# Kernel tuning notes

Hardware: AMD Instinct MI355X
Metric: run time of the kernel (lower is better)

Reference implementation:

```python
import jax, jax.numpy as jnp
import numpy as np

LN_EPS = 1e-5
SN_EPS = 1e-12


def _block(x, W, b, g, be):
    # Linear -> LayerNorm -> CELU, fused as one expression chain
    h = x @ W.T + b
    mu = jnp.mean(h, axis=-1, keepdims=True)
    var = jnp.mean(jnp.square(h - mu), axis=-1, keepdims=True)
    h = (h - mu) * jax.lax.rsqrt(var + LN_EPS) * g + be
    return jax.nn.celu(h)


def _spectral_norm_weight(W, u):
    # One power iteration (torch training-mode behavior), u/v detached.
    v = W.T @ u
    v = v / (jnp.linalg.norm(v) + SN_EPS)
    u2 = W @ v
    u2 = u2 / (jnp.linalg.norm(u2) + SN_EPS)
    sigma = u2 @ (W @ v)
    return W / sigma


def setup_inputs() -> dict:
    key = jax.random.key(0)
    ks = jax.random.split(key, 8)
    B, D = 131072, 512
    sizes = [512, 128, 32, 8]
    inp = {"x": jax.random.normal(ks[0], (B, D), dtype=jnp.float32)}
    fan_in = D
    for i, s in enumerate(sizes, start=1):
        scale = 1.0 / np.sqrt(fan_in)
        inp[f"W{i}"] = jax.random.normal(ks[i], (s, fan_in), dtype=jnp.float32) * scale
        inp[f"b{i}"] = jnp.zeros((s,), dtype=jnp.float32)
        inp[f"g{i}"] = jnp.ones((s,), dtype=jnp.float32)
        inp[f"be{i}"] = jnp.zeros((s,), dtype=jnp.float32)
        fan_in = s
    inp["Wh"] = jax.random.normal(ks[5], (1, 8), dtype=jnp.float32) * (1.0 / np.sqrt(8))
    inp["bh"] = jnp.zeros((1,), dtype=jnp.float32)
    inp["u"] = jax.random.normal(ks[6], (1,), dtype=jnp.float32)
    return inp


def reference(x, W1, b1, g1, be1, W2, b2, g2, be2, W3, b3, g3, be3,
              W4, b4, g4, be4, Wh, bh, u):
    h = _block(x, W1, b1, g1, be1)
    h = _block(h, W2, b2, g2, be2)
    h = _block(h, W3, b3, g3, be3)
    h = _block(h, W4, b4, g4, be4)          # hidden_output: [B, 8]
    Wsn = _spectral_norm_weight(Wh, u)
    return h @ Wsn.T + bh                   # [B, 1]
```

## Files before the change

kernel.cpp:

```cpp
#include <hip/hip_runtime.h>


typedef unsigned short u16;
typedef unsigned int   u32;
typedef __bf16  bf16x8 __attribute__((ext_vector_type(8)));
typedef float   f32x16 __attribute__((ext_vector_type(16)));

__device__ __forceinline__ u16 f2bf(float f) {
    u32 x = __builtin_bit_cast(u32, f);
    x += 0x7FFFu + ((x >> 16) & 1u);
    return (u16)(x >> 16);
}
__device__ __forceinline__ float bfval(u16 h) { return __builtin_bit_cast(float, (u32)h << 16); }
__device__ __forceinline__ u32 pack2(float a, float b) { return (u32)f2bf(a) | ((u32)f2bf(b) << 16); }
__device__ __forceinline__ float celu1(float x) { return x > 0.f ? x : __expf(x) - 1.f; }

#define PB1 0
#define PG1 512
#define PBE1 1024
#define PB2 1536
#define PG2 1664
#define PBE2 1792
#define PB3 1920
#define PG3 1952
#define PBE3 1984
#define PB4 2016
#define PG4 2024
#define PBE4 2032
#define PW4 2040
#define PWH 2296
#define PBH 2304
#define PU  2305
#define NPAR 2306

#define W1F_OFF 0
#define W2F_OFF 262144
#define W3F_OFF 327680
#define W3LF_OFF 331776
#define NGROUPS 41984

__global__ void prep_weights(const float* __restrict__ W1, const float* __restrict__ W2,
                             const float* __restrict__ W3, u16* __restrict__ wsb) {
    const int g = blockIdx.x * 256 + threadIdx.x;
    if (g < 32768) {
        const int l = g & 63, t = (g >> 6) & 15, ksg = g >> 10;
        const int n = t * 32 + (l & 31);
        const int k0 = ksg * 16 + (l >> 5) * 8;
        u16* dst = wsb + W1F_OFF + g * 8;
        const float* src = W1 + n * 512 + k0;
#pragma unroll
        for (int e = 0; e < 8; ++e) dst[e] = f2bf(src[e]);
    } else if (g < 40960) {
        const int h = g - 32768;
        const int l = h & 63, t = (h >> 6) & 3, ksg = h >> 8;
        const int n = t * 32 + (l & 31);
        const int k0 = ksg * 16 + (l >> 5) * 8;
        u16* dst = wsb + W2F_OFF + h * 8;
        const float* src = W2 + n * 512 + k0;
#pragma unroll
        for (int e = 0; e < 8; ++e) dst[e] = f2bf(src[e]);
    } else if (g < 41472) {
        const int h = g - 40960;
        const int l = h & 63, ksg = h >> 6;
        const int n = l & 31;
        const int k0 = ksg * 16 + (l >> 5) * 8;
        u16* dst = wsb + W3F_OFF + h * 8;
        const float* src = W3 + n * 128 + k0;
#pragma unroll
        for (int e = 0; e < 8; ++e) dst[e] = f2bf(src[e]);
    } else {
        const int h = g - 41472;
        const int l = h & 63, ksg = h >> 6;
        const int n = l & 31;
        const int k0 = ksg * 16 + (l >> 5) * 8;
        u16* dst = wsb + W3LF_OFF + h * 8;
        const float* src = W3 + n * 128 + k0;
#pragma unroll
        for (int e = 0; e < 8; ++e) { float w = src[e]; dst[e] = f2bf(w - bfval(f2bf(w))); }
    }
}

__global__ __launch_bounds__(512, 2) void fused_mlp(
    const float* __restrict__ x,
    const u16* __restrict__ W1b, const u16* __restrict__ W2b,
    const u16* __restrict__ W3b, const u16* __restrict__ W3Lb,
    const float* __restrict__ b1, const float* __restrict__ g1, const float* __restrict__ be1,
    const float* __restrict__ b2, const float* __restrict__ g2, const float* __restrict__ be2,
    const float* __restrict__ b3, const float* __restrict__ g3, const float* __restrict__ be3,
    const float* __restrict__ W4, const float* __restrict__ b4, const float* __restrict__ g4,
    const float* __restrict__ be4,
    const float* __restrict__ Wh, const float* __restrict__ bh, const float* __restrict__ uvec,
    float* __restrict__ out)
{
    __shared__ __align__(16) u16 sA[64][72];
    __shared__ __align__(16) u16 sH1[64][520];
    __shared__ __align__(16) u16 sH2[64][136];
    __shared__ __align__(16) u16 sH2L[64][136];
    __shared__ __align__(16) float sH3f[64][36];
    __shared__ __align__(16) float sPS[64][8];
    __shared__ __align__(16) float sPQ[64][8];
    __shared__ float sMu[64], sRs[64];
    __shared__ __align__(16) float sP[NPAR + 2];

    const int tid = threadIdx.x;
    const int row0 = blockIdx.x * 64;
    const int wv = tid >> 6;
    const int lane = tid & 63;
    const int ln = lane & 31;
    const int lh = lane >> 5;

    for (int i = tid; i < NPAR; i += 512) {
        float v;
        if      (i < 512)  v = b1[i];
        else if (i < 1024) v = g1[i - 512];
        else if (i < 1536) v = be1[i - 1024];
        else if (i < 1664) v = b2[i - 1536];
        else if (i < 1792) v = g2[i - 1664];
        else if (i < 1920) v = be2[i - 1792];
        else if (i < 1952) v = b3[i - 1920];
        else if (i < 1984) v = g3[i - 1952];
        else if (i < 2016) v = be3[i - 1984];
        else if (i < 2024) v = b4[i - 2016];
        else if (i < 2032) v = g4[i - 2024];
        else if (i < 2040) v = be4[i - 2032];
        else if (i < 2296) v = W4[i - 2040];
        else if (i < 2304) v = Wh[i - 2296];
        else if (i == 2304) v = bh[0];
        else                v = uvec[0];
        sP[i] = v;
    }

    const int Mt = wv >> 2;
    const int Ng = wv & 3;

    const int sr = tid >> 3;
    const int sc = (tid & 7) * 8;
    const float* xrow = x + (long)(row0 + sr) * 512 + sc;

    float4 pa0 = *(const float4*)(xrow);
    float4 pa1 = *(const float4*)(xrow + 4);
    float4 pb0 = *(const float4*)(xrow + 64);
    float4 pb1 = *(const float4*)(xrow + 68);

    const u16* wq = W1b + (Ng * 4) * 512 + lane * 8;
    bf16x8 Bf[4][4];
#pragma unroll
    for (int s = 0; s < 3; ++s)
#pragma unroll
        for (int nt = 0; nt < 4; ++nt)
            Bf[s][nt] = *(const bf16x8*)(wq + s * 8192 + nt * 512);

    f32x16 acc[4] = {};

#pragma unroll
    for (int c = 0; c < 8; ++c) {
        __syncthreads();
        {
            float4 q0 = (c & 1) ? pb0 : pa0;
            float4 q1 = (c & 1) ? pb1 : pa1;
            uint4 wv4;
            wv4.x = pack2(q0.x, q0.y);
            wv4.y = pack2(q0.z, q0.w);
            wv4.z = pack2(q1.x, q1.y);
            wv4.w = pack2(q1.z, q1.w);
            *(uint4*)(&sA[sr][sc]) = wv4;
        }
        __syncthreads();
        if (c + 2 < 8) {
            const float* nx = xrow + (c + 2) * 64;
            if (c & 1) { pb0 = *(const float4*)(nx); pb1 = *(const float4*)(nx + 4); }
            else       { pa0 = *(const float4*)(nx); pa1 = *(const float4*)(nx + 4); }
        }
#pragma unroll
        for (int ks = 0; ks < 4; ++ks) {
            const int ksg = c * 4 + ks;
            const int slot = ksg & 3;
            if (ksg + 3 < 32) {
                const int ps = (ksg + 3) & 3;
                const u16* np = wq + (ksg + 3) * 8192;
                Bf[ps][0] = *(const bf16x8*)(np);
                Bf[ps][1] = *(const bf16x8*)(np + 512);
                Bf[ps][2] = *(const bf16x8*)(np + 1024);
                Bf[ps][3] = *(const bf16x8*)(np + 1536);
            }
            bf16x8 af = *(const bf16x8*)(&sA[Mt * 32 + ln][ks * 16 + lh * 8]);
            acc[0] = __builtin_amdgcn_mfma_f32_32x32x16_bf16(af, Bf[slot][0], acc[0], 0, 0, 0);
            acc[1] = __builtin_amdgcn_mfma_f32_32x32x16_bf16(af, Bf[slot][1], acc[1], 0, 0, 0);
            acc[2] = __builtin_amdgcn_mfma_f32_32x32x16_bf16(af, Bf[slot][2], acc[2], 0, 0, 0);
            acc[3] = __builtin_amdgcn_mfma_f32_32x32x16_bf16(af, Bf[slot][3], acc[3], 0, 0, 0);
        }
    }

#pragma unroll
    for (int nt = 0; nt < 4; ++nt) {
        const float bb = sP[PB1 + (Ng * 4 + nt) * 32 + ln];
#pragma unroll
        for (int rg = 0; rg < 16; ++rg) acc[nt][rg] += bb;
    }
#pragma unroll
    for (int rg = 0; rg < 16; ++rg) {
        float s = acc[0][rg] + acc[1][rg] + acc[2][rg] + acc[3][rg];
        float q = acc[0][rg] * acc[0][rg] + acc[1][rg] * acc[1][rg]
                + acc[2][rg] * acc[2][rg] + acc[3][rg] * acc[3][rg];
#pragma unroll
        for (int m = 1; m < 32; m <<= 1) { s += __shfl_xor(s, m, 64); q += __shfl_xor(q, m, 64); }
        if (ln == 0) {
            const int row = Mt * 32 + (rg & 3) + 8 * (rg >> 2) + 4 * lh;
            sPS[row][Ng] = s; sPQ[row][Ng] = q;
        }
    }
    __syncthreads();
    if (tid < 64) {
        float s = sPS[tid][0] + sPS[tid][1] + sPS[tid][2] + sPS[tid][3];
        float q = sPQ[tid][0] + sPQ[tid][1] + sPQ[tid][2] + sPQ[tid][3];
        const float mu = s * (1.f / 512.f);
        const float var = q * (1.f / 512.f) - mu * mu;
        sMu[tid] = mu; sRs[tid] = rsqrtf(var + 1e-5f);
    }
    __syncthreads();
    {
        float gg[4], ee[4];
#pragma unroll
        for (int nt = 0; nt < 4; ++nt) {
            const int col = (Ng * 4 + nt) * 32 + ln;
            gg[nt] = sP[PG1 + col]; ee[nt] = sP[PBE1 + col];
        }
#pragma unroll
        for (int rg = 0; rg < 16; ++rg) {
            const int row = Mt * 32 + (rg & 3) + 8 * (rg >> 2) + 4 * lh;
            const float mu = sMu[row], rs = sRs[row];
#pragma unroll
            for (int nt = 0; nt < 4; ++nt) {
                const int col = (Ng * 4 + nt) * 32 + ln;
                const float hn = (acc[nt][rg] - mu) * rs * gg[nt] + ee[nt];
                sH1[row][col] = f2bf(celu1(hn));
            }
        }
    }
    __syncthreads();

    float v2[16];
    {
        const int Mt2 = wv >> 2;
        const int Nt2 = wv & 3;
        const u16* w2q = W2b + Nt2 * 512 + lane * 8;
        bf16x8 W2f[4];
#pragma unroll
        for (int s = 0; s < 4; ++s) W2f[s] = *(const bf16x8*)(w2q + s * 2048);

        f32x16 a2 = {}, a2b = {};
        const u16* h1p = &sH1[Mt2 * 32 + ln][lh * 8];
#pragma unroll
        for (int ksg = 0; ksg < 32; ++ksg) {
            const int slot = ksg & 3;
            bf16x8 af = *(const bf16x8*)(h1p + ksg * 16);
            if (ksg & 1) a2b = __builtin_amdgcn_mfma_f32_32x32x16_bf16(af, W2f[slot], a2b, 0, 0, 0);
            else         a2  = __builtin_amdgcn_mfma_f32_32x32x16_bf16(af, W2f[slot], a2, 0, 0, 0);
            if (ksg + 4 < 32) W2f[slot] = *(const bf16x8*)(w2q + (ksg + 4) * 2048);
        }
        const float bb = sP[PB2 + Nt2 * 32 + ln];
#pragma unroll
        for (int rg = 0; rg < 16; ++rg) v2[rg] = a2[rg] + a2b[rg] + bb;
#pragma unroll
        for (int rg = 0; rg < 16; ++rg) {
            float s = v2[rg], q = v2[rg] * v2[rg];
#pragma unroll
            for (int m = 1; m < 32; m <<= 1) { s += __shfl_xor(s, m, 64); q += __shfl_xor(q, m, 64); }
            if (ln == 0) {
                const int row = Mt2 * 32 + (rg & 3) + 8 * (rg >> 2) + 4 * lh;
                sPS[row][Nt2] = s; sPQ[row][Nt2] = q;
            }
        }
    }
    __syncthreads();
    if (tid < 64) {
        float s = sPS[tid][0] + sPS[tid][1] + sPS[tid][2] + sPS[tid][3];
        float q = sPQ[tid][0] + sPQ[tid][1] + sPQ[tid][2] + sPQ[tid][3];
        const float mu = s * (1.f / 128.f);
        const float var = q * (1.f / 128.f) - mu * mu;
        sMu[tid] = mu; sRs[tid] = rsqrtf(var + 1e-5f);
    }
    __syncthreads();
    {
        const int Mt2 = wv >> 2;
        const int Nt2 = wv & 3;
        const int col = Nt2 * 32 + ln;
        const float gg = sP[PG2 + col], ee = sP[PBE2 + col];
#pragma unroll
        for (int rg = 0; rg < 16; ++rg) {
            const int row = Mt2 * 32 + (rg & 3) + 8 * (rg >> 2) + 4 * lh;
            const float hn = (v2[rg] - sMu[row]) * sRs[row] * gg + ee;
            const float a = celu1(hn);
            const u16 hi = f2bf(a);
            sH2[row][col] = hi;
            sH2L[row][col] = f2bf(a - bfval(hi));
        }
    }
    __syncthreads();

    if (wv < 2) {
        f32x16 a3 = {};
        const u16* w3q  = W3b  + lane * 8;
        const u16* w3lq = W3Lb + lane * 8;
        const u16* h2p  = &sH2 [wv * 32 + ln][lh * 8];
        const u16* h2lp = &sH2L[wv * 32 + ln][lh * 8];
#pragma unroll
        for (int ks = 0; ks < 8; ++ks) {
            bf16x8 fa_h = *(const bf16x8*)(h2p  + ks * 16);
            bf16x8 fa_l = *(const bf16x8*)(h2lp + ks * 16);
            bf16x8 fb_h = *(const bf16x8*)(w3q  + ks * 512);
            bf16x8 fb_l = *(const bf16x8*)(w3lq + ks * 512);
            a3 = __builtin_amdgcn_mfma_f32_32x32x16_bf16(fa_h, fb_h, a3, 0, 0, 0);
            a3 = __builtin_amdgcn_mfma_f32_32x32x16_bf16(fa_h, fb_l, a3, 0, 0, 0);
            a3 = __builtin_amdgcn_mfma_f32_32x32x16_bf16(fa_l, fb_h, a3, 0, 0, 0);
        }
        const float bb = sP[PB3 + ln];
        const float g3v = sP[PG3 + ln], e3v = sP[PBE3 + ln];
#pragma unroll
        for (int rg = 0; rg < 16; ++rg) {
            const float v = a3[rg] + bb;
            float s = v, q = v * v;
#pragma unroll
            for (int m = 1; m < 32; m <<= 1) { s += __shfl_xor(s, m, 64); q += __shfl_xor(q, m, 64); }
            const float mu = s * (1.f / 32.f);
            const float rs = rsqrtf(q * (1.f / 32.f) - mu * mu + 1e-5f);
            const int row = wv * 32 + (rg & 3) + 8 * (rg >> 2) + 4 * lh;
            sH3f[row][ln] = celu1((v - mu) * rs * g3v + e3v);
        }
    }
    __syncthreads();

    if (tid < 256) {
        const int r = tid & 63, og = tid >> 6;
        float h[32];
        const float4* hp = (const float4*)(&sH3f[r][0]);
#pragma unroll
        for (int j = 0; j < 8; ++j) {
            float4 t = hp[j];
            h[j * 4 + 0] = t.x; h[j * 4 + 1] = t.y; h[j * 4 + 2] = t.z; h[j * 4 + 3] = t.w;
        }
#pragma unroll
        for (int oo = 0; oo < 2; ++oo) {
            const int o = og * 2 + oo;
            float a = sP[PB4 + o];
            const float* w4 = &sP[PW4 + o * 32];
#pragma unroll
            for (int k = 0; k < 32; ++k) a += h[k] * w4[k];
            sPS[r][o] = a;
        }
    }
    __syncthreads();

    if (tid < 64) {
        float v[8];
        float s = 0.f, q = 0.f;
#pragma unroll
        for (int o = 0; o < 8; ++o) { v[o] = sPS[tid][o]; s += v[o]; q += v[o] * v[o]; }
        const float mu = s * 0.125f;
        const float var = q * 0.125f - mu * mu;
        const float rs = rsqrtf(var + 1e-5f);

        float wh[8];
        const float u0 = sP[PU];
        float nv = 0.f;
#pragma unroll
        for (int o = 0; o < 8; ++o) { wh[o] = sP[PWH + o]; float t = wh[o] * u0; nv += t * t; }
        nv = sqrtf(nv);
        const float inv = 1.f / (nv + 1e-12f);
        float s2 = 0.f;
#pragma unroll
        for (int o = 0; o < 8; ++o) s2 += wh[o] * (wh[o] * u0 * inv);
        const float u2 = s2 / (fabsf(s2) + 1e-12f);
        const float sigma = u2 * s2;
        const float isg = 1.f / sigma;

        float y = sP[PBH];
#pragma unroll
        for (int o = 0; o < 8; ++o) {
            const float hn = (v[o] - mu) * rs * sP[PG4 + o] + sP[PBE4 + o];
            y += celu1(hn) * wh[o] * isg;
        }
        out[row0 + tid] = y;
    }
}

extern "C" void kernel_launch(void* const* d_in, const int* in_sizes, int n_in,
                              void* d_out, int out_size, void* d_ws, size_t ws_size,
                              hipStream_t stream) {
    const float* x   = (const float*)d_in[0];
    const float* W1  = (const float*)d_in[1];
    const float* b1  = (const float*)d_in[2];
    const float* g1  = (const float*)d_in[3];
    const float* be1 = (const float*)d_in[4];
    const float* W2  = (const float*)d_in[5];
    const float* b2  = (const float*)d_in[6];
    const float* g2  = (const float*)d_in[7];
    const float* be2 = (const float*)d_in[8];
    const float* W3  = (const float*)d_in[9];
    const float* b3  = (const float*)d_in[10];
    const float* g3  = (const float*)d_in[11];
    const float* be3 = (const float*)d_in[12];
    const float* W4  = (const float*)d_in[13];
    const float* b4  = (const float*)d_in[14];
    const float* g4  = (const float*)d_in[15];
    const float* be4 = (const float*)d_in[16];
    const float* Wh  = (const float*)d_in[17];
    const float* bh  = (const float*)d_in[18];
    const float* u   = (const float*)d_in[19];
    float* out = (float*)d_out;
    u16* wsb = (u16*)d_ws;

    prep_weights<<<dim3(NGROUPS / 256), dim3(256), 0, stream>>>(W1, W2, W3, wsb);

    const int rows = in_sizes[0] / 512;
    fused_mlp<<<dim3(rows / 64), dim3(512), 0, stream>>>(
        x, wsb + W1F_OFF, wsb + W2F_OFF, wsb + W3F_OFF, wsb + W3LF_OFF,
        b1, g1, be1, b2, g2, be2, b3, g3, be3,
        W4, b4, g4, be4, Wh, bh, u, out);
}
```

Baseline: 604.9 us.

## Make fused MLP persistent with register-prefetched x tiles across iterations

The kernel becomes persistent: 256 blocks each loop over T 64-row tiles. The next tile of x is prefetched into registers as packed bf16 while the current tile's layer-1 MFMA runs, and the whole 64x512 tile is staged into a shared buffer reused for the H1 activations. Layer 1 is re-tiled so each of the 8 waves owns 64 output columns across both row halves, removing the per-chunk double syncs. This trades grid-level parallelism and occupancy (256 blocks, extra registers for px) for overlap of global loads with compute and fewer barriers. It assumes the row count divides evenly by 64*256.

```diff
diff --git a/kernel.cpp b/kernel.cpp
--- a/kernel.cpp
+++ b/kernel.cpp
@@ -90,24 +90,35 @@
     const float* __restrict__ W4, const float* __restrict__ b4, const float* __restrict__ g4,
     const float* __restrict__ be4,
     const float* __restrict__ Wh, const float* __restrict__ bh, const float* __restrict__ uvec,
-    float* __restrict__ out)
+    float* __restrict__ out, const int T)
 {
-    __shared__ __align__(16) u16 sA[64][72];
-    __shared__ __align__(16) u16 sH1[64][520];
+    __shared__ __align__(16) u16 sXH[64][520];
     __shared__ __align__(16) u16 sH2[64][136];
     __shared__ __align__(16) u16 sH2L[64][136];
     __shared__ __align__(16) float sH3f[64][36];
     __shared__ __align__(16) float sPS[64][8];
     __shared__ __align__(16) float sPQ[64][8];
-    __shared__ float sMu[64], sRs[64];
+    __shared__ __align__(8)  float2 sMR[64];
     __shared__ __align__(16) float sP[NPAR + 2];
 
     const int tid = threadIdx.x;
-    const int row0 = blockIdx.x * 64;
     const int wv = tid >> 6;
     const int lane = tid & 63;
     const int ln = lane & 31;
     const int lh = lane >> 5;
+    const int Ng = wv;
+
+    const long base = (long)blockIdx.x * T * 64 * 512;
+
+    uint2 px[16];
+    {
+        const float4* xp = (const float4*)(x + base) + tid;
+#pragma unroll
+        for (int j = 0; j < 16; ++j) {
+            float4 q = xp[j * 512];
+            px[j] = make_uint2(pack2(q.x, q.y), pack2(q.z, q.w));
+        }
+    }
 
     for (int i = tid; i < NPAR; i += 512) {
         float v;
@@ -130,257 +141,249 @@
         sP[i] = v;
     }
 
-    const int Mt = wv >> 2;
-    const int Ng = wv & 3;
-
-    const int sr = tid >> 3;
-    const int sc = (tid & 7) * 8;
-    const float* xrow = x + (long)(row0 + sr) * 512 + sc;
-
-    float4 pa0 = *(const float4*)(xrow);
-    float4 pa1 = *(const float4*)(xrow + 4);
-    float4 pb0 = *(const float4*)(xrow + 64);
-    float4 pb1 = *(const float4*)(xrow + 68);
-
-    const u16* wq = W1b + (Ng * 4) * 512 + lane * 8;
-    bf16x8 Bf[4][4];
-#pragma unroll
-    for (int s = 0; s < 3; ++s)
-#pragma unroll
-        for (int nt = 0; nt < 4; ++nt)
-            Bf[s][nt] = *(const bf16x8*)(wq + s * 8192 + nt * 512);
-
-    f32x16 acc[4] = {};
-
-#pragma unroll
-    for (int c = 0; c < 8; ++c) {
-        __syncthreads();
-        {
-            float4 q0 = (c & 1) ? pb0 : pa0;
-            float4 q1 = (c & 1) ? pb1 : pa1;
-            uint4 wv4;
-            wv4.x = pack2(q0.x, q0.y);
-            wv4.y = pack2(q0.z, q0.w);
-            wv4.z = pack2(q1.x, q1.y);
-            wv4.w = pack2(q1.z, q1.w);
-            *(uint4*)(&sA[sr][sc]) = wv4;
-        }
-        __syncthreads();
-        if (c + 2 < 8) {
-            const float* nx = xrow + (c + 2) * 64;
-            if (c & 1) { pb0 = *(const float4*)(nx); pb1 = *(const float4*)(nx + 4); }
-            else       { pa0 = *(const float4*)(nx); pa1 = *(const float4*)(nx + 4); }
-        }
-#pragma unroll
-        for (int ks = 0; ks < 4; ++ks) {
-            const int ksg = c * 4 + ks;
-            const int slot = ksg & 3;
-            if (ksg + 3 < 32) {
-                const int ps = (ksg + 3) & 3;
-                const u16* np = wq + (ksg + 3) * 8192;
-                Bf[ps][0] = *(const bf16x8*)(np);
-                Bf[ps][1] = *(const bf16x8*)(np + 512);
-                Bf[ps][2] = *(const bf16x8*)(np + 1024);
-                Bf[ps][3] = *(const bf16x8*)(np + 1536);
-            }
-            bf16x8 af = *(const bf16x8*)(&sA[Mt * 32 + ln][ks * 16 + lh * 8]);
-            acc[0] = __builtin_amdgcn_mfma_f32_32x32x16_bf16(af, Bf[slot][0], acc[0], 0, 0, 0);
-            acc[1] = __builtin_amdgcn_mfma_f32_32x32x16_bf16(af, Bf[slot][1], acc[1], 0, 0, 0);
-            acc[2] = __builtin_amdgcn_mfma_f32_32x32x16_bf16(af, Bf[slot][2], acc[2], 0, 0, 0);
-            acc[3] = __builtin_amdgcn_mfma_f32_32x32x16_bf16(af, Bf[slot][3], acc[3], 0, 0, 0);
-        }
-    }
-
-#pragma unroll
-    for (int nt = 0; nt < 4; ++nt) {
-        const float bb = sP[PB1 + (Ng * 4 + nt) * 32 + ln];
-#pragma unroll
-        for (int rg = 0; rg < 16; ++rg) acc[nt][rg] += bb;
-    }
-#pragma unroll
-    for (int rg = 0; rg < 16; ++rg) {
-        float s = acc[0][rg] + acc[1][rg] + acc[2][rg] + acc[3][rg];
-        float q = acc[0][rg] * acc[0][rg] + acc[1][rg] * acc[1][rg]
-                + acc[2][rg] * acc[2][rg] + acc[3][rg] * acc[3][rg];
-#pragma unroll
-        for (int m = 1; m < 32; m <<= 1) { s += __shfl_xor(s, m, 64); q += __shfl_xor(q, m, 64); }
-        if (ln == 0) {
-            const int row = Mt * 32 + (rg & 3) + 8 * (rg >> 2) + 4 * lh;
-            sPS[row][Ng] = s; sPQ[row][Ng] = q;
-        }
-    }
-    __syncthreads();
-    if (tid < 64) {
-        float s = sPS[tid][0] + sPS[tid][1] + sPS[tid][2] + sPS[tid][3];
-        float q = sPQ[tid][0] + sPQ[tid][1] + sPQ[tid][2] + sPQ[tid][3];
-        const float mu = s * (1.f / 512.f);
-        const float var = q * (1.f / 512.f) - mu * mu;
-        sMu[tid] = mu; sRs[tid] = rsqrtf(var + 1e-5f);
-    }
-    __syncthreads();
-    {
-        float gg[4], ee[4];
-#pragma unroll
-        for (int nt = 0; nt < 4; ++nt) {
-            const int col = (Ng * 4 + nt) * 32 + ln;
-            gg[nt] = sP[PG1 + col]; ee[nt] = sP[PBE1 + col];
-        }
+#pragma unroll 1
+    for (int t = 0; t < T; ++t) {
+        const long row0 = (long)blockIdx.x * T * 64 + (long)t * 64;
+
+        {
+            const int r0 = tid >> 7;
+            const int c4 = (tid & 127) * 4;
+#pragma unroll
+            for (int j = 0; j < 16; ++j)
+                *(uint2*)(&sXH[j * 4 + r0][c4]) = px[j];
+        }
+        __syncthreads();
+
+        f32x16 acc[2][2] = {};
+        {
+            const u16* wq = W1b + (Ng * 2) * 512 + lane * 8;
+            bf16x8 Bf[4][2];
+#pragma unroll
+            for (int s = 0; s < 3; ++s) {
+                Bf[s][0] = *(const bf16x8*)(wq + s * 8192);
+                Bf[s][1] = *(const bf16x8*)(wq + s * 8192 + 512);
+            }
+#pragma unroll
+            for (int ksg = 0; ksg < 32; ++ksg) {
+                const int slot = ksg & 3;
+                if (ksg + 3 < 32) {
+                    const int ps = (ksg + 3) & 3;
+                    const u16* np = wq + (ksg + 3) * 8192;
+                    Bf[ps][0] = *(const bf16x8*)(np);
+                    Bf[ps][1] = *(const bf16x8*)(np + 512);
+                }
+                bf16x8 a0 = *(const bf16x8*)(&sXH[ln][ksg * 16 + lh * 8]);
+                bf16x8 a1 = *(const bf16x8*)(&sXH[32 + ln][ksg * 16 + lh * 8]);
+                acc[0][0] = __builtin_amdgcn_mfma_f32_32x32x16_bf16(a0, Bf[slot][0], acc[0][0], 0, 0, 0);
+                acc[0][1] = __builtin_amdgcn_mfma_f32_32x32x16_bf16(a0, Bf[slot][1], acc[0][1], 0, 0, 0);
+                acc[1][0] = __builtin_amdgcn_mfma_f32_32x32x16_bf16(a1, Bf[slot][0], acc[1][0], 0, 0, 0);
+                acc[1][1] = __builtin_amdgcn_mfma_f32_32x32x16_bf16(a1, Bf[slot][1], acc[1][1], 0, 0, 0);
+            }
+        }
+
+        if (t + 1 < T) {
+            const float4* xp = (const float4*)(x + base + (long)(t + 1) * 64 * 512) + tid;
+#pragma unroll
+            for (int j = 0; j < 16; ++j) {
+                float4 q = xp[j * 512];
+                px[j] = make_uint2(pack2(q.x, q.y), pack2(q.z, q.w));
+            }
+        }
+
+        {
+            const float b0 = sP[PB1 + Ng * 64 + ln];
+            const float b1c = sP[PB1 + Ng * 64 + 32 + ln];
+#pragma unroll
+            for (int rg = 0; rg < 16; ++rg) {
+                acc[0][0][rg] += b0; acc[0][1][rg] += b1c;
+                acc[1][0][rg] += b0; acc[1][1][rg] += b1c;
+            }
+        }
+#pragma unroll
+        for (int mt = 0; mt < 2; ++mt)
 #pragma unroll
         for (int rg = 0; rg < 16; ++rg) {
-            const int row = Mt * 32 + (rg & 3) + 8 * (rg >> 2) + 4 * lh;
-            const float mu = sMu[row], rs = sRs[row];
-#pragma unroll
-            for (int nt = 0; nt < 4; ++nt) {
-                const int col = (Ng * 4 + nt) * 32 + ln;
-                const float hn = (acc[nt][rg] - mu) * rs * gg[nt] + ee[nt];
-                sH1[row][col] = f2bf(celu1(hn));
-            }
-        }
-    }
-    __syncthreads();
-
-    float v2[16];
-    {
-        const int Mt2 = wv >> 2;
-        const int Nt2 = wv & 3;
-        const u16* w2q = W2b + Nt2 * 512 + lane * 8;
-        bf16x8 W2f[4];
-#pragma unroll
-        for (int s = 0; s < 4; ++s) W2f[s] = *(const bf16x8*)(w2q + s * 2048);
-
-        f32x16 a2 = {}, a2b = {};
-        const u16* h1p = &sH1[Mt2 * 32 + ln][lh * 8];
-#pragma unroll
-        for (int ksg = 0; ksg < 32; ++ksg) {
-            const int slot = ksg & 3;
-            bf16x8 af = *(const bf16x8*)(h1p + ksg * 16);
-            if (ksg & 1) a2b = __builtin_amdgcn_mfma_f32_32x32x16_bf16(af, W2f[slot], a2b, 0, 0, 0);
-            else         a2  = __builtin_amdgcn_mfma_f32_32x32x16_bf16(af, W2f[slot], a2, 0, 0, 0);
-            if (ksg + 4 < 32) W2f[slot] = *(const bf16x8*)(w2q + (ksg + 4) * 2048);
-        }
-        const float bb = sP[PB2 + Nt2 * 32 + ln];
-#pragma unroll
-        for (int rg = 0; rg < 16; ++rg) v2[rg] = a2[rg] + a2b[rg] + bb;
-#pragma unroll
-        for (int rg = 0; rg < 16; ++rg) {
-            float s = v2[rg], q = v2[rg] * v2[rg];
+            float s = acc[mt][0][rg] + acc[mt][1][rg];
+            float q = acc[mt][0][rg] * acc[mt][0][rg] + acc[mt][1][rg] * acc[mt][1][rg];
 #pragma unroll
             for (int m = 1; m < 32; m <<= 1) { s += __shfl_xor(s, m, 64); q += __shfl_xor(q, m, 64); }
             if (ln == 0) {
+                const int row = mt * 32 + (rg & 3) + 8 * (rg >> 2) + 4 * lh;
+                sPS[row][Ng] = s; sPQ[row][Ng] = q;
+            }
+        }
+        __syncthreads();
+        if (tid < 64) {
+            float s = 0.f, q = 0.f;
+#pragma unroll
+            for (int j = 0; j < 8; ++j) { s += sPS[tid][j]; q += sPQ[tid][j]; }
+            const float mu = s * (1.f / 512.f);
+            const float var = q * (1.f / 512.f) - mu * mu;
+            sMR[tid] = make_float2(mu, rsqrtf(var + 1e-5f));
+        }
+        __syncthreads();
+        {
+            const float g0 = sP[PG1 + Ng * 64 + ln];
+            const float gA = sP[PG1 + Ng * 64 + 32 + ln];
+            const float e0 = sP[PBE1 + Ng * 64 + ln];
+            const float eA = sP[PBE1 + Ng * 64 + 32 + ln];
+#pragma unroll
+            for (int mt = 0; mt < 2; ++mt)
+#pragma unroll
+            for (int rg = 0; rg < 16; ++rg) {
+                const int row = mt * 32 + (rg & 3) + 8 * (rg >> 2) + 4 * lh;
+                const float2 mr = sMR[row];
+                const float h0 = (acc[mt][0][rg] - mr.x) * mr.y * g0 + e0;
+                const float h1v = (acc[mt][1][rg] - mr.x) * mr.y * gA + eA;
+                sXH[row][Ng * 64 + ln] = f2bf(celu1(h0));
+                sXH[row][Ng * 64 + 32 + ln] = f2bf(celu1(h1v));
+            }
+        }
+        __syncthreads();
+
+        float v2[16];
+        {
+            const int Mt2 = wv >> 2;
+            const int Nt2 = wv & 3;
+            const u16* w2q = W2b + Nt2 * 512 + lane * 8;
+            bf16x8 W2f[4];
+#pragma unroll
+            for (int s = 0; s < 4; ++s) W2f[s] = *(const bf16x8*)(w2q + s * 2048);
+            f32x16 a2 = {}, a2b = {};
+            const u16* h1p = &sXH[Mt2 * 32 + ln][lh * 8];
+#pragma unroll
+            for (int ksg = 0; ksg < 32; ++ksg) {
+                const int slot = ksg & 3;
+                bf16x8 af = *(const bf16x8*)(h1p + ksg * 16);
+                if (ksg & 1) a2b = __builtin_amdgcn_mfma_f32_32x32x16_bf16(af, W2f[slot], a2b, 0, 0, 0);
+                else         a2  = __builtin_amdgcn_mfma_f32_32x32x16_bf16(af, W2f[slot], a2, 0, 0, 0);
+                if (ksg + 4 < 32) W2f[slot] = *(const bf16x8*)(w2q + (ksg + 4) * 2048);
+            }
+            const float bb = sP[PB2 + Nt2 * 32 + ln];
+#pragma unroll
+            for (int rg = 0; rg < 16; ++rg) v2[rg] = a2[rg] + a2b[rg] + bb;
+#pragma unroll
+            for (int rg = 0; rg < 16; ++rg) {
+                float s = v2[rg], q = v2[rg] * v2[rg];
+#pragma unroll
+                for (int m = 1; m < 32; m <<= 1) { s += __shfl_xor(s, m, 64); q += __shfl_xor(q, m, 64); }
+                if (ln == 0) {
+                    const int row = Mt2 * 32 + (rg & 3) + 8 * (rg >> 2) + 4 * lh;
+                    sPS[row][Nt2] = s; sPQ[row][Nt2] = q;
+                }
+            }
+        }
+        __syncthreads();
+        if (tid < 64) {
+            float s = sPS[tid][0] + sPS[tid][1] + sPS[tid][2] + sPS[tid][3];
+            float q = sPQ[tid][0] + sPQ[tid][1] + sPQ[tid][2] + sPQ[tid][3];
+            const float mu = s * (1.f / 128.f);
+            const float var = q * (1.f / 128.f) - mu * mu;
+            sMR[tid] = make_float2(mu, rsqrtf(var + 1e-5f));
+        }
+        __syncthreads();
+        {
+            const int Mt2 = wv >> 2;
+            const int Nt2 = wv & 3;
+            const int col = Nt2 * 32 + ln;
+            const float gg = sP[PG2 + col], ee = sP[PBE2 + col];
+#pragma unroll
+            for (int rg = 0; rg < 16; ++rg) {
                 const int row = Mt2 * 32 + (rg & 3) + 8 * (rg >> 2) + 4 * lh;
-                sPS[row][Nt2] = s; sPQ[row][Nt2] = q;
-            }
-        }
-    }
-    __syncthreads();
-    if (tid < 64) {
-        float s = sPS[tid][0] + sPS[tid][1] + sPS[tid][2] + sPS[tid][3];
-        float q = sPQ[tid][0] + sPQ[tid][1] + sPQ[tid][2] + sPQ[tid][3];
-        const float mu = s * (1.f / 128.f);
-        const float var = q * (1.f / 128.f) - mu * mu;
-        sMu[tid] = mu; sRs[tid] = rsqrtf(var + 1e-5f);
-    }
-    __syncthreads();
-    {
-        const int Mt2 = wv >> 2;
-        const int Nt2 = wv & 3;
-        const int col = Nt2 * 32 + ln;
-        const float gg = sP[PG2 + col], ee = sP[PBE2 + col];
-#pragma unroll
-        for (int rg = 0; rg < 16; ++rg) {
-            const int row = Mt2 * 32 + (rg & 3) + 8 * (rg >> 2) + 4 * lh;
-            const float hn = (v2[rg] - sMu[row]) * sRs[row] * gg + ee;
-            const float a = celu1(hn);
-            const u16 hi = f2bf(a);
-            sH2[row][col] = hi;
-            sH2L[row][col] = f2bf(a - bfval(hi));
-        }
-    }
-    __syncthreads();
-
-    if (wv < 2) {
-        f32x16 a3 = {};
-        const u16* w3q  = W3b  + lane * 8;
-        const u16* w3lq = W3Lb + lane * 8;
-        const u16* h2p  = &sH2 [wv * 32 + ln][lh * 8];
-        const u16* h2lp = &sH2L[wv * 32 + ln][lh * 8];
-#pragma unroll
-        for (int ks = 0; ks < 8; ++ks) {
-            bf16x8 fa_h = *(const bf16x8*)(h2p  + ks * 16);
-            bf16x8 fa_l = *(const bf16x8*)(h2lp + ks * 16);
-            bf16x8 fb_h = *(const bf16x8*)(w3q  + ks * 512);
-            bf16x8 fb_l = *(const bf16x8*)(w3lq + ks * 512);
-            a3 = __builtin_amdgcn_mfma_f32_32x32x16_bf16(fa_h, fb_h, a3, 0, 0, 0);
-            a3 = __builtin_amdgcn_mfma_f32_32x32x16_bf16(fa_h, fb_l, a3, 0, 0, 0);
-            a3 = __builtin_amdgcn_mfma_f32_32x32x16_bf16(fa_l, fb_h, a3, 0, 0, 0);
-        }
-        const float bb = sP[PB3 + ln];
-        const float g3v = sP[PG3 + ln], e3v = sP[PBE3 + ln];
-#pragma unroll
-        for (int rg = 0; rg < 16; ++rg) {
-            const float v = a3[rg] + bb;
-            float s = v, q = v * v;
-#pragma unroll
-            for (int m = 1; m < 32; m <<= 1) { s += __shfl_xor(s, m, 64); q += __shfl_xor(q, m, 64); }
-            const float mu = s * (1.f / 32.f);
-            const float rs = rsqrtf(q * (1.f / 32.f) - mu * mu + 1e-5f);
-            const int row = wv * 32 + (rg & 3) + 8 * (rg >> 2) + 4 * lh;
-            sH3f[row][ln] = celu1((v - mu) * rs * g3v + e3v);
-        }
-    }
-    __syncthreads();
-
-    if (tid < 256) {
-        const int r = tid & 63, og = tid >> 6;
-        float h[32];
-        const float4* hp = (const float4*)(&sH3f[r][0]);
-#pragma unroll
-        for (int j = 0; j < 8; ++j) {
-            float4 t = hp[j];
-            h[j * 4 + 0] = t.x; h[j * 4 + 1] = t.y; h[j * 4 + 2] = t.z; h[j * 4 + 3] = t.w;
-        }
-#pragma unroll
-        for (int oo = 0; oo < 2; ++oo) {
-            const int o = og * 2 + oo;
-            float a = sP[PB4 + o];
-            const float* w4 = &sP[PW4 + o * 32];
-#pragma unroll
-            for (int k = 0; k < 32; ++k) a += h[k] * w4[k];
-            sPS[r][o] = a;
-        }
-    }
-    __syncthreads();
-
-    if (tid < 64) {
-        float v[8];
-        float s = 0.f, q = 0.f;
-#pragma unroll
-        for (int o = 0; o < 8; ++o) { v[o] = sPS[tid][o]; s += v[o]; q += v[o] * v[o]; }
-        const float mu = s * 0.125f;
-        const float var = q * 0.125f - mu * mu;
-        const float rs = rsqrtf(var + 1e-5f);
-
-        float wh[8];
-        const float u0 = sP[PU];
-        float nv = 0.f;
-#pragma unroll
-        for (int o = 0; o < 8; ++o) { wh[o] = sP[PWH + o]; float t = wh[o] * u0; nv += t * t; }
-        nv = sqrtf(nv);
-        const float inv = 1.f / (nv + 1e-12f);
-        float s2 = 0.f;
-#pragma unroll
-        for (int o = 0; o < 8; ++o) s2 += wh[o] * (wh[o] * u0 * inv);
-        const float u2 = s2 / (fabsf(s2) + 1e-12f);
-        const float sigma = u2 * s2;
-        const float isg = 1.f / sigma;
-
-        float y = sP[PBH];
-#pragma unroll
-        for (int o = 0; o < 8; ++o) {
-            const float hn = (v[o] - mu) * rs * sP[PG4 + o] + sP[PBE4 + o];
-            y += celu1(hn) * wh[o] * isg;
-        }
-        out[row0 + tid] = y;
+                const float2 mr = sMR[row];
+                const float hn = (v2[rg] - mr.x) * mr.y * gg + ee;
+                const float a = celu1(hn);
+                const u16 hi = f2bf(a);
+                sH2[row][col] = hi;
+                sH2L[row][col] = f2bf(a - bfval(hi));
+            }
+        }
+        __syncthreads();
+
+        if (wv < 2) {
+            f32x16 a3 = {};
+            const u16* w3q  = W3b  + lane * 8;
+            const u16* w3lq = W3Lb + lane * 8;
+            const u16* h2p  = &sH2 [wv * 32 + ln][lh * 8];
+            const u16* h2lp = &sH2L[wv * 32 + ln][lh * 8];
+#pragma unroll
+            for (int ks = 0; ks < 8; ++ks) {
+                bf16x8 fa_h = *(const bf16x8*)(h2p  + ks * 16);
+                bf16x8 fa_l = *(const bf16x8*)(h2lp + ks * 16);
+                bf16x8 fb_h = *(const bf16x8*)(w3q  + ks * 512);
+                bf16x8 fb_l = *(const bf16x8*)(w3lq + ks * 512);
+                a3 = __builtin_amdgcn_mfma_f32_32x32x16_bf16(fa_h, fb_h, a3, 0, 0, 0);
+                a3 = __builtin_amdgcn_mfma_f32_32x32x16_bf16(fa_h, fb_l, a3, 0, 0, 0);
+                a3 = __builtin_amdgcn_mfma_f32_32x32x16_bf16(fa_l, fb_h, a3, 0, 0, 0);
+            }
+            const float bb = sP[PB3 + ln];
+            const float g3v = sP[PG3 + ln], e3v = sP[PBE3 + ln];
+#pragma unroll
+            for (int rg = 0; rg < 16; ++rg) {
+                const float v = a3[rg] + bb;
+                float s = v, q = v * v;
+#pragma unroll
+                for (int m = 1; m < 32; m <<= 1) { s += __shfl_xor(s, m, 64); q += __shfl_xor(q, m, 64); }
+                const float mu = s * (1.f / 32.f);
+                const float rs = rsqrtf(q * (1.f / 32.f) - mu * mu + 1e-5f);
+                const int row = wv * 32 + (rg & 3) + 8 * (rg >> 2) + 4 * lh;
+                sH3f[row][ln] = celu1((v - mu) * rs * g3v + e3v);
+            }
+        }
+        __syncthreads();
+
+        if (tid < 256) {
+            const int r = tid & 63, og = tid >> 6;
+            float h[32];
+            const float4* hp = (const float4*)(&sH3f[r][0]);
+#pragma unroll
+            for (int j = 0; j < 8; ++j) {
+                float4 tv = hp[j];
+                h[j * 4 + 0] = tv.x; h[j * 4 + 1] = tv.y; h[j * 4 + 2] = tv.z; h[j * 4 + 3] = tv.w;
+            }
+#pragma unroll
+            for (int oo = 0; oo < 2; ++oo) {
+                const int o = og * 2 + oo;
+                float a = sP[PB4 + o];
+                const float* w4 = &sP[PW4 + o * 32];
+#pragma unroll
+                for (int k = 0; k < 32; ++k) a += h[k] * w4[k];
+                sPS[r][o] = a;
+            }
+        }
+        __syncthreads();
+
+        if (tid < 64) {
+            float v[8];
+            float s = 0.f, q = 0.f;
+#pragma unroll
+            for (int o = 0; o < 8; ++o) { v[o] = sPS[tid][o]; s += v[o]; q += v[o] * v[o]; }
+            const float mu = s * 0.125f;
+            const float var = q * 0.125f - mu * mu;
+            const float rs = rsqrtf(var + 1e-5f);
+
+            float wh[8];
+            const float u0 = sP[PU];
+            float nv = 0.f;
+#pragma unroll
+            for (int o = 0; o < 8; ++o) { wh[o] = sP[PWH + o]; float tt = wh[o] * u0; nv += tt * tt; }
+            nv = sqrtf(nv);
+            const float inv = 1.f / (nv + 1e-12f);
+            float s2 = 0.f;
+#pragma unroll
+            for (int o = 0; o < 8; ++o) s2 += wh[o] * (wh[o] * u0 * inv);
+            const float u2 = s2 / (fabsf(s2) + 1e-12f);
+            const float sigma = u2 * s2;
+            const float isg = 1.f / sigma;
+
+            float y = sP[PBH];
+#pragma unroll
+            for (int o = 0; o < 8; ++o) {
+                const float hn = (v[o] - mu) * rs * sP[PG4 + o] + sP[PBE4 + o];
+                y += celu1(hn) * wh[o] * isg;
+            }
+            out[row0 + tid] = y;
+        }
     }
 }
 
@@ -413,8 +416,10 @@
     prep_weights<<<dim3(NGROUPS / 256), dim3(256), 0, stream>>>(W1, W2, W3, wsb);
 
     const int rows = in_sizes[0] / 512;
-    fused_mlp<<<dim3(rows / 64), dim3(512), 0, stream>>>(
+    const int blocks = 256;
+    const int T = rows / 64 / blocks;
+    fused_mlp<<<dim3(blocks), dim3(512), 0, stream>>>(
         x, wsb + W1F_OFF, wsb + W2F_OFF, wsb + W3F_OFF, wsb + W3LF_OFF,
         b1, g1, be1, b2, g2, be2, b3, g3, be3,
-        W4, b4, g4, be4, Wh, bh, u, out);
+        W4, b4, g4, be4, Wh, bh, u, out, T);
 }
```

Measured after the change: 798.1 us. 1.32x slower.
